# Optimization experiments

Measured on AMD Instinct MI355X. Metric: run time of the kernel, lower is better.

## Reference

```python
import jax, jax.numpy as jnp
import numpy as np

N, K, C, OUT = 2048, 14, 512, 512
SCALE = 4.0
BN_EPS = 1e-5


def _edge_lists(k):
    # pairs i<j with i,j != k-1 and adj[i,j] > 0 (adj is fully connected ones)
    ei, ej = [], []
    for i in range(k - 1):
        for j in range(i + 1, k - 1):
            ei.append(i)
            ej.append(j)
    return np.asarray(ei, np.int32), np.asarray(ej, np.int32)


def setup_inputs() -> dict:
    key = jax.random.key(0)
    k0, k1, k2, k3 = jax.random.split(key, 4)
    ei, ej = _edge_lists(K)
    std = 0.02
    return {
        "inputs": jax.random.normal(k0, (N, K, C), dtype=jnp.float32),
        "adj": jnp.ones((K, K), dtype=jnp.float32),
        "edge_i": jnp.asarray(ei),
        "edge_j": jnp.asarray(ej),
        "gamma": jnp.ones((C,), dtype=jnp.float32),
        "beta": jnp.zeros((C,), dtype=jnp.float32),
        "w_direct": jax.random.normal(k1, (C,), dtype=jnp.float32) * std,
        "W_merged": jax.random.normal(k2, (OUT, C), dtype=jnp.float32) * std,
        "W_orig": jax.random.normal(k3, (OUT, C), dtype=jnp.float32) * std,
    }


def reference(inputs, adj, edge_i, edge_j, gamma, beta, w_direct, W_merged, W_orig):
    n, k, c = inputs.shape
    # --- learn_adj ---
    global_feat = inputs[:, k - 1 : k, :]                      # [N,1,c]
    distances = jnp.abs(inputs - global_feat)                  # [N,k,c]
    # pairwise gaps only on the static edge list (i<j, non-global, adj>0)
    gap = 15.0 * (distances[:, edge_i, :] - distances[:, edge_j, :])  # [N,E,c]
    # BatchNorm1d over channel c, batch stats over (N, E), biased variance
    mean = jnp.mean(gap, axis=(0, 1))
    var = jnp.mean(jnp.square(gap - mean), axis=(0, 1))
    bn = (gap - mean) * (gamma / jnp.sqrt(var + BN_EPS)) + beta        # [N,E,c]
    a = jax.nn.sigmoid(SCALE * jnp.einsum("nec,c->ne", bn, w_direct))  # [N,E]
    adj2 = jnp.ones((n, k, k), dtype=inputs.dtype)
    adj2 = adj2.at[:, edge_i, edge_j].set(2.0 * a)
    adj2 = adj2.at[:, edge_j, edge_i].set(2.0 * (1.0 - a))
    new_adj = adj2 * adj[None, :, :]
    norm = jnp.sum(jnp.abs(new_adj), axis=2, keepdims=True)    # L1 row norm
    new_adj = new_adj / jnp.maximum(norm, 1e-12)
    # --- graph conv ---
    agg = jnp.einsum("nij,njc->nic", new_adj, inputs)          # [N,k,c]
    merged = jax.nn.relu(jnp.einsum("nkc,oc->nko", agg, W_merged))
    original = jnp.einsum("nkc,oc->nko", inputs, W_orig)
    return merged + original
```

## Files before the change

### kernel.cpp

```cpp
#include <hip/hip_runtime.h>
#include <stdint.h>

#define K_NODES 14
#define C_DIM   512
#define OUT_DIM 512
#define N_EDGE  78

typedef float  f32x4  __attribute__((ext_vector_type(4)));
typedef __bf16 bf16x8 __attribute__((ext_vector_type(8)));

__device__ __forceinline__ unsigned short f2bf(float f) {
    unsigned int u = __builtin_bit_cast(unsigned int, f);
    unsigned int r = (u + 0x7fffu + ((u >> 16) & 1u)) >> 16;
    return (unsigned short)r;
}
__device__ __forceinline__ float bf2f(unsigned short s) {
    return __builtin_bit_cast(float, (unsigned int)s << 16);
}

__device__ __forceinline__ void async16(const void* g, void* l) {
    __builtin_amdgcn_global_load_lds(
        (const __attribute__((address_space(1))) unsigned int*)g,
        (__attribute__((address_space(3))) unsigned int*)l, 16, 0, 0);
}

__global__ __launch_bounds__(512) void stats_partial(
    const float* __restrict__ x, float* __restrict__ part,
    unsigned short* __restrict__ xbf, int n_per_block,
    const float* __restrict__ Wm, const float* __restrict__ Wo,
    unsigned short* __restrict__ wmbf, unsigned short* __restrict__ wobf,
    float* __restrict__ bconst)
{
    int c  = threadIdx.x;
    int n0 = blockIdx.x * n_per_block;
    float s_sum = 0.f, s_sq = 0.f;
    for (int nn = 0; nn < n_per_block; ++nn) {
        size_t base = (size_t)(n0 + nn) * K_NODES * C_DIM + c;
        const float* xb = x + base;
        unsigned short* xo = xbf + base;
        float g = xb[13 * C_DIM];
        xo[13 * C_DIM] = f2bf(g);
        float S1 = 0.f, S2 = 0.f, Sw = 0.f;
        #pragma unroll
        for (int k = 0; k < 13; ++k) {
            float v = xb[k * C_DIM];
            xo[k * C_DIM] = f2bf(v);
            float d = fabsf(v - g);
            S1 += d; S2 += d * d; Sw += (float)(12 - 2 * k) * d;
        }
        s_sum += 15.f * Sw;
        s_sq  += 225.f * (13.f * S2 - S1 * S1);
    }
    part[(size_t)blockIdx.x * 1024 + c]       = s_sum;
    part[(size_t)blockIdx.x * 1024 + 512 + c] = s_sq;
    {
        int i0 = blockIdx.x * 1024 + c;
        wmbf[i0]       = f2bf(Wm[i0]);
        wmbf[i0 + 512] = f2bf(Wm[i0 + 512]);
        wobf[i0]       = f2bf(Wo[i0]);
        wobf[i0 + 512] = f2bf(Wo[i0 + 512]);
    }
    if (blockIdx.x == 0 && c == 0) *bconst = 0.f;
}

__global__ __launch_bounds__(1024) void finalize_stats(
    const float* __restrict__ part, float inv_ne,
    const float* __restrict__ gamma, const float* __restrict__ beta,
    const float* __restrict__ wdir, float* __restrict__ u, float* __restrict__ bconst)
{
    int c = threadIdx.x & 511;
    int h = threadIdx.x >> 9;
    float s = 0.f, q = 0.f;
    for (int b = h * 128; b < h * 128 + 128; b += 8) {
        #pragma unroll
        for (int t = 0; t < 8; ++t) {
            s += part[(size_t)(b + t) * 1024 + c];
            q += part[(size_t)(b + t) * 1024 + 512 + c];
        }
    }
    __shared__ float sh_s[512], sh_q[512], red[512];
    if (h == 0) { sh_s[c] = s; sh_q[c] = q; }
    __syncthreads();
    if (h == 1) { sh_s[c] += s; sh_q[c] += q; }
    __syncthreads();
    if (h == 0) {
        float mean = sh_s[c] * inv_ne;
        float var  = sh_q[c] * inv_ne - mean * mean;
        float sc   = gamma[c] / sqrtf(var + 1e-5f);
        u[c] = sc * wdir[c];
        red[c] = (beta[c] - mean * sc) * wdir[c];
    }
    __syncthreads();
    for (int st = 256; st > 0; st >>= 1) {
        if (threadIdx.x < st) red[threadIdx.x] += red[threadIdx.x + st];
        __syncthreads();
    }
    if (threadIdx.x == 0) *bconst = red[0];
}

__global__ __launch_bounds__(512) void fuse_graph(
    const unsigned short* __restrict__ xbf, const float* __restrict__ adj,
    const int* __restrict__ ei, const int* __restrict__ ej,
    const float* __restrict__ u, const float* __restrict__ bconst,
    unsigned short* __restrict__ aggbf)
{
    __shared__ float Dl[13];
    __shared__ float Wl[K_NODES * K_NODES];
    __shared__ float rnorm[K_NODES];
    int n = blockIdx.x, c = threadIdx.x;
    size_t base = (size_t)n * K_NODES * C_DIM + c;

    float xv[K_NODES];
    #pragma unroll
    for (int k = 0; k < K_NODES; ++k) xv[k] = bf2f(xbf[base + k * C_DIM]);

    if (c < 13) Dl[c] = 0.f;
    __syncthreads();

    float g  = xv[13];
    float uc = u[c];
    #pragma unroll
    for (int k = 0; k < 13; ++k) {
        float val = fabsf(xv[k] - g) * uc;
        #pragma unroll
        for (int off = 32; off > 0; off >>= 1) val += __shfl_down(val, off, 64);
        if ((c & 63) == 0) atomicAdd(&Dl[k], val);
    }
    __syncthreads();

    if (c < K_NODES * K_NODES) Wl[c] = 1.f;
    __syncthreads();
    if (c < N_EDGE) {
        float z = 4.0f * (15.f * (Dl[ei[c]] - Dl[ej[c]]) + *bconst);
        float a = 1.f / (1.f + expf(-z));
        Wl[ei[c] * K_NODES + ej[c]] = 2.f * a;
        Wl[ej[c] * K_NODES + ei[c]] = 2.f * (1.f - a);
    }
    __syncthreads();
    if (c < K_NODES * K_NODES) Wl[c] *= adj[c];
    __syncthreads();
    if (c < K_NODES) {
        float s = 0.f;
        #pragma unroll
        for (int j = 0; j < K_NODES; ++j) s += fabsf(Wl[c * K_NODES + j]);
        rnorm[c] = fmaxf(s, 1e-12f);
    }
    __syncthreads();
    if (c < K_NODES * K_NODES) Wl[c] /= rnorm[c / K_NODES];
    __syncthreads();

    #pragma unroll
    for (int i = 0; i < K_NODES; ++i) {
        float s = 0.f;
        #pragma unroll
        for (int j = 0; j < K_NODES; ++j) s += Wl[i * K_NODES + j] * xv[j];
        aggbf[base + i * C_DIM] = f2bf(s);
    }
}

#define TM 128
#define TN 128
#define BK 64

__global__ __launch_bounds__(256) void gemm_fused(
    const unsigned short* __restrict__ Aagg, const unsigned short* __restrict__ Axin,
    const unsigned short* __restrict__ Bwm,  const unsigned short* __restrict__ Bwo,
    float* __restrict__ out)
{
    __shared__ unsigned short lA[TM * BK];
    __shared__ unsigned short lB[TN * BK];
    int tid  = threadIdx.x;
    int lane = tid & 63;
    int wave = tid >> 6;
    int wr = wave >> 1, wc = wave & 1;
    int bm = blockIdx.x * TM;
    int bn = blockIdx.y * TN;

    f32x4 acc[4][4];
    #pragma unroll
    for (int i = 0; i < 4; ++i)
        #pragma unroll
        for (int j = 0; j < 4; ++j) acc[i][j] = (f32x4){0.f, 0.f, 0.f, 0.f};

    int lrow = lane & 15;
    int xorv = lane & 7;
    int srow  = tid >> 3;
    int lcu   = ((tid & 7) ^ (srow & 7)) * 8;

    #pragma unroll
    for (int pass = 0; pass < 2; ++pass) {
        const unsigned short* A = pass ? Axin : Aagg;
        const unsigned short* B = pass ? Bwo  : Bwm;
        for (int kb = 0; kb < C_DIM; kb += BK) {
            __syncthreads();
            #pragma unroll
            for (int it = 0; it < 4; ++it) {
                int row = it * 32 + srow;
                async16(A + (size_t)(bm + row) * C_DIM + kb + lcu,
                        &lA[(size_t)(it * 256 + wave * 64) * 8]);
                async16(B + (size_t)(bn + row) * C_DIM + kb + lcu,
                        &lB[(size_t)(it * 256 + wave * 64) * 8]);
            }
            __syncthreads();
            #pragma unroll
            for (int ks = 0; ks < 2; ++ks) {
                int pchunk = ((ks * 4 + (lane >> 4)) ^ xorv) * 8;
                bf16x8 af[4], bfr[4];
                #pragma unroll
                for (int i = 0; i < 4; ++i)
                    af[i] = *(const bf16x8*)&lA[(wr * 64 + i * 16 + lrow) * BK + pchunk];
                #pragma unroll
                for (int j = 0; j < 4; ++j)
                    bfr[j] = *(const bf16x8*)&lB[(wc * 64 + j * 16 + lrow) * BK + pchunk];
                #pragma unroll
                for (int i = 0; i < 4; ++i)
                    #pragma unroll
                    for (int j = 0; j < 4; ++j)
                        acc[i][j] = __builtin_amdgcn_mfma_f32_16x16x32_bf16(
                            af[i], bfr[j], acc[i][j], 0, 0, 0);
            }
        }
        if (pass == 0) {
            #pragma unroll
            for (int i = 0; i < 4; ++i)
                #pragma unroll
                for (int j = 0; j < 4; ++j)
                    #pragma unroll
                    for (int r = 0; r < 4; ++r)
                        acc[i][j][r] = fmaxf(acc[i][j][r], 0.f);
        }
    }

    int orow0 = bm + wr * 64 + (lane >> 4) * 4;
    int ocol0 = bn + wc * 64 + (lane & 15);
    #pragma unroll
    for (int i = 0; i < 4; ++i)
        #pragma unroll
        for (int j = 0; j < 4; ++j)
            #pragma unroll
            for (int r = 0; r < 4; ++r)
                out[(size_t)(orow0 + i * 16 + r) * OUT_DIM + (ocol0 + j * 16)] = acc[i][j][r];
}

extern "C" void kernel_launch(void* const* d_in, const int* in_sizes, int n_in,
                              void* d_out, int out_size, void* d_ws, size_t ws_size,
                              hipStream_t stream)
{
    const float* x     = (const float*)d_in[0];
    const float* adj   = (const float*)d_in[1];
    const int*   ei    = (const int*)d_in[2];
    const int*   ej    = (const int*)d_in[3];
    const float* gamma = (const float*)d_in[4];
    const float* beta  = (const float*)d_in[5];
    const float* wdir  = (const float*)d_in[6];
    const float* Wm    = (const float*)d_in[7];
    const float* Wo    = (const float*)d_in[8];
    float* out = (float*)d_out;

    int N = in_sizes[0] / (K_NODES * C_DIM);
    int M = N * K_NODES;

    float* ws_f   = (float*)d_ws;
    float* u      = ws_f + 1024;
    float* bconst = ws_f + 1536;
    float* part   = ws_f + 2048;
    char*  wsb    = (char*)d_ws;
    size_t off    = (size_t)(2048 + 256 * 1024) * sizeof(float);
    unsigned short* wmbf  = (unsigned short*)(wsb + off);  off += (size_t)OUT_DIM * C_DIM * 2;
    unsigned short* wobf  = (unsigned short*)(wsb + off);  off += (size_t)OUT_DIM * C_DIM * 2;
    unsigned short* xbf   = (unsigned short*)(wsb + off);  off += (size_t)M * C_DIM * 2;
    unsigned short* aggbf = (unsigned short*)(wsb + off);

    const int stats_blocks = 256;
    int n_per_block = N / stats_blocks;
    float inv_ne = 1.0f / ((float)N * (float)N_EDGE);

    hipLaunchKernelGGL(stats_partial, dim3(stats_blocks), dim3(512), 0, stream,
                       x, part, xbf, n_per_block, Wm, Wo, wmbf, wobf, bconst);
    hipLaunchKernelGGL(finalize_stats, dim3(1), dim3(1024), 0, stream,
                       part, inv_ne, gamma, beta, wdir, u, bconst);
    hipLaunchKernelGGL(fuse_graph, dim3(N), dim3(512), 0, stream,
                       xbf, adj, ei, ej, u, bconst, aggbf);
    hipLaunchKernelGGL(gemm_fused, dim3(M / TM, OUT_DIM / TN), dim3(256), 0, stream,
                       aggbf, xbf, wmbf, wobf, out);
}
```

Before: 204.2 us.

## Vectorize stats and graph-fuse kernels, one wave per sample in fuse_graph

stats_partial now loads four channels per thread as float4 and writes packed bf16, with four sample groups per block reduced through shared memory. fuse_graph assigns one 64-lane wave per sample, with each lane handling eight channels through 16-byte loads and stores. The atomic reduction becomes a wave xor-shuffle, and the row normalization is folded into the output scale as a reciprocal multiply. The aim is to cut memory transaction count and block-wide syncs in the two preprocessing kernels, at the cost of more registers per thread.

```diff
diff --git a/kernel.cpp b/kernel.cpp
--- a/kernel.cpp
+++ b/kernel.cpp
@@ -28,39 +28,51 @@
     const float* __restrict__ x, float* __restrict__ part,
     unsigned short* __restrict__ xbf, int n_per_block,
     const float* __restrict__ Wm, const float* __restrict__ Wo,
-    unsigned short* __restrict__ wmbf, unsigned short* __restrict__ wobf,
-    float* __restrict__ bconst)
-{
-    int c  = threadIdx.x;
+    unsigned short* __restrict__ wmbf, unsigned short* __restrict__ wobf)
+{
+    int t  = threadIdx.x;
+    int q  = t & 127;
+    int sn = t >> 7;
     int n0 = blockIdx.x * n_per_block;
-    float s_sum = 0.f, s_sq = 0.f;
-    for (int nn = 0; nn < n_per_block; ++nn) {
-        size_t base = (size_t)(n0 + nn) * K_NODES * C_DIM + c;
-        const float* xb = x + base;
-        unsigned short* xo = xbf + base;
-        float g = xb[13 * C_DIM];
-        xo[13 * C_DIM] = f2bf(g);
-        float S1 = 0.f, S2 = 0.f, Sw = 0.f;
+    float as0=0.f,as1=0.f,as2=0.f,as3=0.f;
+    float aq0=0.f,aq1=0.f,aq2=0.f,aq3=0.f;
+    for (int nn = sn; nn < n_per_block; nn += 4) {
+        size_t base = (size_t)(n0 + nn) * K_NODES * C_DIM + q * 4;
+        f32x4 g = *(const f32x4*)(x + base + 13 * C_DIM);
+        ushort4 gb; gb.x=f2bf(g.x); gb.y=f2bf(g.y); gb.z=f2bf(g.z); gb.w=f2bf(g.w);
+        *(ushort4*)(xbf + base + 13 * C_DIM) = gb;
+        float S10=0,S11=0,S12=0,S13=0, S20=0,S21=0,S22=0,S23=0, Sw0=0,Sw1=0,Sw2=0,Sw3=0;
         #pragma unroll
         for (int k = 0; k < 13; ++k) {
-            float v = xb[k * C_DIM];
-            xo[k * C_DIM] = f2bf(v);
-            float d = fabsf(v - g);
-            S1 += d; S2 += d * d; Sw += (float)(12 - 2 * k) * d;
-        }
-        s_sum += 15.f * Sw;
-        s_sq  += 225.f * (13.f * S2 - S1 * S1);
-    }
-    part[(size_t)blockIdx.x * 1024 + c]       = s_sum;
-    part[(size_t)blockIdx.x * 1024 + 512 + c] = s_sq;
-    {
-        int i0 = blockIdx.x * 1024 + c;
-        wmbf[i0]       = f2bf(Wm[i0]);
-        wmbf[i0 + 512] = f2bf(Wm[i0 + 512]);
-        wobf[i0]       = f2bf(Wo[i0]);
-        wobf[i0 + 512] = f2bf(Wo[i0 + 512]);
-    }
-    if (blockIdx.x == 0 && c == 0) *bconst = 0.f;
+            f32x4 v = *(const f32x4*)(x + base + k * C_DIM);
+            ushort4 vb; vb.x=f2bf(v.x); vb.y=f2bf(v.y); vb.z=f2bf(v.z); vb.w=f2bf(v.w);
+            *(ushort4*)(xbf + base + k * C_DIM) = vb;
+            float wk = (float)(12 - 2 * k);
+            float d0=fabsf(v.x-g.x), d1=fabsf(v.y-g.y), d2=fabsf(v.z-g.z), d3=fabsf(v.w-g.w);
+            S10+=d0; S11+=d1; S12+=d2; S13+=d3;
+            S20+=d0*d0; S21+=d1*d1; S22+=d2*d2; S23+=d3*d3;
+            Sw0+=wk*d0; Sw1+=wk*d1; Sw2+=wk*d2; Sw3+=wk*d3;
+        }
+        as0 += 15.f*Sw0; as1 += 15.f*Sw1; as2 += 15.f*Sw2; as3 += 15.f*Sw3;
+        aq0 += 225.f*(13.f*S20 - S10*S10); aq1 += 225.f*(13.f*S21 - S11*S11);
+        aq2 += 225.f*(13.f*S22 - S12*S12); aq3 += 225.f*(13.f*S23 - S13*S13);
+    }
+    __shared__ f32x4 redS[4][128];
+    __shared__ f32x4 redQ[4][128];
+    redS[sn][q] = (f32x4){as0, as1, as2, as3};
+    redQ[sn][q] = (f32x4){aq0, aq1, aq2, aq3};
+    __syncthreads();
+    if (sn == 0) {
+        f32x4 s = redS[0][q] + redS[1][q] + redS[2][q] + redS[3][q];
+        f32x4 z = redQ[0][q] + redQ[1][q] + redQ[2][q] + redQ[3][q];
+        *(f32x4*)(part + (size_t)blockIdx.x * 1024 + q * 4)       = s;
+        *(f32x4*)(part + (size_t)blockIdx.x * 1024 + 512 + q * 4) = z;
+    }
+    int i0 = blockIdx.x * 1024 + t;
+    wmbf[i0]       = f2bf(Wm[i0]);
+    wmbf[i0 + 512] = f2bf(Wm[i0 + 512]);
+    wobf[i0]       = f2bf(Wo[i0]);
+    wobf[i0 + 512] = f2bf(Wo[i0 + 512]);
 }
 
 __global__ __launch_bounds__(1024) void finalize_stats(
@@ -71,9 +83,9 @@
     int c = threadIdx.x & 511;
     int h = threadIdx.x >> 9;
     float s = 0.f, q = 0.f;
-    for (int b = h * 128; b < h * 128 + 128; b += 8) {
-        #pragma unroll
-        for (int t = 0; t < 8; ++t) {
+    for (int b = h * 128; b < h * 128 + 128; b += 16) {
+        #pragma unroll
+        for (int t = 0; t < 16; ++t) {
             s += part[(size_t)(b + t) * 1024 + c];
             q += part[(size_t)(b + t) * 1024 + 512 + c];
         }
@@ -98,63 +110,82 @@
     if (threadIdx.x == 0) *bconst = red[0];
 }
 
-__global__ __launch_bounds__(512) void fuse_graph(
+__global__ __launch_bounds__(256) void fuse_graph(
     const unsigned short* __restrict__ xbf, const float* __restrict__ adj,
     const int* __restrict__ ei, const int* __restrict__ ej,
     const float* __restrict__ u, const float* __restrict__ bconst,
     unsigned short* __restrict__ aggbf)
 {
-    __shared__ float Dl[13];
-    __shared__ float Wl[K_NODES * K_NODES];
-    __shared__ float rnorm[K_NODES];
-    int n = blockIdx.x, c = threadIdx.x;
-    size_t base = (size_t)n * K_NODES * C_DIM + c;
-
-    float xv[K_NODES];
-    #pragma unroll
-    for (int k = 0; k < K_NODES; ++k) xv[k] = bf2f(xbf[base + k * C_DIM]);
-
-    if (c < 13) Dl[c] = 0.f;
-    __syncthreads();
-
-    float g  = xv[13];
-    float uc = u[c];
+    __shared__ float WL[4][196];
+    __shared__ float DlL[4][16];
+    __shared__ float invL[4][16];
+    int wv = threadIdx.x >> 6, lane = threadIdx.x & 63;
+    int n = blockIdx.x * 4 + wv;
+    size_t base = (size_t)n * K_NODES * C_DIM + lane * 8;
+
+    float xf[K_NODES][8];
+    #pragma unroll
+    for (int k = 0; k < K_NODES; ++k) {
+        uint4 raw = *(const uint4*)(xbf + base + k * C_DIM);
+        unsigned int w0=raw.x, w1=raw.y, w2=raw.z, w3=raw.w;
+        xf[k][0]=bf2f(w0&0xffff); xf[k][1]=bf2f(w0>>16);
+        xf[k][2]=bf2f(w1&0xffff); xf[k][3]=bf2f(w1>>16);
+        xf[k][4]=bf2f(w2&0xffff); xf[k][5]=bf2f(w2>>16);
+        xf[k][6]=bf2f(w3&0xffff); xf[k][7]=bf2f(w3>>16);
+    }
+    f32x4 u0 = *(const f32x4*)(u + lane * 8);
+    f32x4 u1 = *(const f32x4*)(u + lane * 8 + 4);
+    float uc[8] = {u0.x,u0.y,u0.z,u0.w,u1.x,u1.y,u1.z,u1.w};
+
     #pragma unroll
     for (int k = 0; k < 13; ++k) {
-        float val = fabsf(xv[k] - g) * uc;
-        #pragma unroll
-        for (int off = 32; off > 0; off >>= 1) val += __shfl_down(val, off, 64);
-        if ((c & 63) == 0) atomicAdd(&Dl[k], val);
-    }
-    __syncthreads();
-
-    if (c < K_NODES * K_NODES) Wl[c] = 1.f;
-    __syncthreads();
-    if (c < N_EDGE) {
-        float z = 4.0f * (15.f * (Dl[ei[c]] - Dl[ej[c]]) + *bconst);
+        float p = 0.f;
+        #pragma unroll
+        for (int j = 0; j < 8; ++j) p += fabsf(xf[k][j] - xf[13][j]) * uc[j];
+        #pragma unroll
+        for (int off = 1; off < 64; off <<= 1) p += __shfl_xor(p, off, 64);
+        if (lane == 0) DlL[wv][k] = p;
+    }
+    __syncthreads();
+
+    #pragma unroll
+    for (int e = 0; e < 4; ++e) {
+        int idx = e * 64 + lane;
+        if (idx < 196) WL[wv][idx] = adj[idx];
+    }
+    __syncthreads();
+    for (int e = lane; e < N_EDGE; e += 64) {
+        int ii = ei[e], jj = ej[e];
+        float z = 4.0f * (15.f * (DlL[wv][ii] - DlL[wv][jj]) + *bconst);
         float a = 1.f / (1.f + expf(-z));
-        Wl[ei[c] * K_NODES + ej[c]] = 2.f * a;
-        Wl[ej[c] * K_NODES + ei[c]] = 2.f * (1.f - a);
-    }
-    __syncthreads();
-    if (c < K_NODES * K_NODES) Wl[c] *= adj[c];
-    __syncthreads();
-    if (c < K_NODES) {
+        WL[wv][ii * K_NODES + jj] *= 2.f * a;
+        WL[wv][jj * K_NODES + ii] *= 2.f * (1.f - a);
+    }
+    __syncthreads();
+    if (lane < K_NODES) {
         float s = 0.f;
         #pragma unroll
-        for (int j = 0; j < K_NODES; ++j) s += fabsf(Wl[c * K_NODES + j]);
-        rnorm[c] = fmaxf(s, 1e-12f);
-    }
-    __syncthreads();
-    if (c < K_NODES * K_NODES) Wl[c] /= rnorm[c / K_NODES];
+        for (int j = 0; j < K_NODES; ++j) s += fabsf(WL[wv][lane * K_NODES + j]);
+        invL[wv][lane] = 1.f / fmaxf(s, 1e-12f);
+    }
     __syncthreads();
 
     #pragma unroll
     for (int i = 0; i < K_NODES; ++i) {
-        float s = 0.f;
-        #pragma unroll
-        for (int j = 0; j < K_NODES; ++j) s += Wl[i * K_NODES + j] * xv[j];
-        aggbf[base + i * C_DIM] = f2bf(s);
+        float s[8] = {0,0,0,0,0,0,0,0};
+        #pragma unroll
+        for (int j = 0; j < K_NODES; ++j) {
+            float w = WL[wv][i * K_NODES + j];
+            #pragma unroll
+            for (int c = 0; c < 8; ++c) s[c] += w * xf[j][c];
+        }
+        float wi = invL[wv][i];
+        uint4 r;
+        r.x = (unsigned int)f2bf(s[0]*wi) | ((unsigned int)f2bf(s[1]*wi) << 16);
+        r.y = (unsigned int)f2bf(s[2]*wi) | ((unsigned int)f2bf(s[3]*wi) << 16);
+        r.z = (unsigned int)f2bf(s[4]*wi) | ((unsigned int)f2bf(s[5]*wi) << 16);
+        r.w = (unsigned int)f2bf(s[6]*wi) | ((unsigned int)f2bf(s[7]*wi) << 16);
+        *(uint4*)(aggbf + base + i * C_DIM) = r;
     }
 }
 
@@ -276,10 +307,10 @@
     float inv_ne = 1.0f / ((float)N * (float)N_EDGE);
 
     hipLaunchKernelGGL(stats_partial, dim3(stats_blocks), dim3(512), 0, stream,
-                       x, part, xbf, n_per_block, Wm, Wo, wmbf, wobf, bconst);
+                       x, part, xbf, n_per_block, Wm, Wo, wmbf, wobf);
     hipLaunchKernelGGL(finalize_stats, dim3(1), dim3(1024), 0, stream,
                        part, inv_ne, gamma, beta, wdir, u, bconst);
-    hipLaunchKernelGGL(fuse_graph, dim3(N), dim3(512), 0, stream,
+    hipLaunchKernelGGL(fuse_graph, dim3(N / 4), dim3(256), 0, stream,
                        xbf, adj, ei, ej, u, bconst, aggbf);
     hipLaunchKernelGGL(gemm_fused, dim3(M / TM, OUT_DIM / TN), dim3(256), 0, stream,
                        aggbf, xbf, wmbf, wobf, out);
```

After: 193.5 us. 5.2% less time.
